# Performance work log

Measured on AMD Instinct MI355X. Metric: run time of the kernel, lower is better.

## Reference

```python
import jax, jax.numpy as jnp
import numpy as np

N = 50000
E = 800000
P = 400000
D_IN = 128
D_HID = 128


def setup_inputs() -> dict:
    key = jax.random.key(0)
    k = jax.random.split(key, 7)
    edge_index = jax.random.randint(k[0], (2, E), 0, N, dtype=jnp.int32)
    edge_pairs = jax.random.randint(k[1], (2, P), 0, N, dtype=jnp.int32)
    emb = jax.random.normal(k[2], (N, D_IN), dtype=jnp.float32)
    W1 = jax.random.normal(k[3], (D_IN, D_HID), dtype=jnp.float32) * (1.0 / np.sqrt(D_IN))
    b1 = jnp.zeros((D_HID,), dtype=jnp.float32)
    W2 = jax.random.normal(k[4], (D_HID, D_HID), dtype=jnp.float32) * (1.0 / np.sqrt(D_HID))
    b2 = jnp.zeros((D_HID,), dtype=jnp.float32)
    return {"edge_index": edge_index, "edge_pairs": edge_pairs, "emb": emb,
            "W1": W1, "b1": b1, "W2": W2, "b2": b2}


def gcn_conv(x, W, b, src, dst):
    """PyG GCNConv: add self-loops, symmetric deg^-1/2 normalization,
    linear transform, scatter-add aggregation into destination nodes."""
    n = x.shape[0]
    loop = jnp.arange(n, dtype=src.dtype)
    s = jnp.concatenate([src, loop])  # [E+N]
    d = jnp.concatenate([dst, loop])
    deg = jax.ops.segment_sum(jnp.ones_like(d, dtype=x.dtype), d, num_segments=n)
    dinv = jnp.where(deg > 0, jax.lax.rsqrt(jnp.maximum(deg, 1e-12)), 0.0)
    norm = dinv[s] * dinv[d]  # [E+N]
    h = x @ W  # [N, out]
    msg = h[s] * norm[:, None]  # gather + scale
    out = jax.ops.segment_sum(msg, d, num_segments=n)  # scatter-add
    return out + b


def reference(edge_index, edge_pairs, emb, W1, b1, W2, b2):
    src, dst = edge_index[0], edge_index[1]
    # encode (eval mode: dropout is identity)
    z = jax.nn.relu(gcn_conv(emb, W1, b1, src, dst))
    z = gcn_conv(z, W2, b2, src, dst)
    # decode: dot product per candidate pair
    return jnp.sum(z[edge_pairs[0]] * z[edge_pairs[1]], axis=1)  # [P]
```

## Files before the change

kernel.cpp:

```cpp
#include <hip/hip_runtime.h>


typedef __attribute__((ext_vector_type(8))) short short8;
typedef __attribute__((ext_vector_type(4))) float floatx4;

#define STAGE_G 128

__device__ __forceinline__ unsigned short f2bf(float f) {
    union { float f; unsigned int u; } v; v.f = f;
    unsigned int u = v.u;
    u += 0x7fffu + ((u >> 16) & 1u);
    return (unsigned short)(u >> 16);
}

__device__ __forceinline__ unsigned int pack2(float a, float b) {
    return (unsigned int)f2bf(a) | ((unsigned int)f2bf(b) << 16);
}

__device__ __forceinline__ float4 cvt4(unsigned int lo, unsigned int hi) {
    float4 f;
    f.x = __uint_as_float(lo << 16);
    f.y = __uint_as_float(lo & 0xffff0000u);
    f.z = __uint_as_float(hi << 16);
    f.w = __uint_as_float(hi & 0xffff0000u);
    return f;
}


__global__ __launch_bounds__(256) void block_hist_kernel(const int* __restrict__ dst,
                                                         int* __restrict__ bhist,
                                                         int E, int NB) {
    __shared__ int bh[1024];
    int t = threadIdx.x, g = blockIdx.x;
    for (int b = t; b < NB; b += 256) bh[b] = 0;
    __syncthreads();
    int chunk = (E + gridDim.x - 1) / gridDim.x;
    int lo = g * chunk, hi = min(lo + chunk, E);
    for (int i = lo + t; i < hi; i += 256) atomicAdd(&bh[dst[i] >> 6], 1);
    __syncthreads();
    for (int b = t; b < NB; b += 256) bhist[g * NB + b] = bh[b];
}

__global__ __launch_bounds__(128) void s1_scan_blocks(int* __restrict__ bhist,
                                                      int* __restrict__ T, int NB) {
    __shared__ int s[2][128];
    int b = blockIdx.x, t = threadIdx.x;
    int v = bhist[t * NB + b];
    int cur = 0;
    s[0][t] = v;
    __syncthreads();
#pragma unroll
    for (int off = 1; off < 128; off <<= 1) {
        int nxt = cur ^ 1;
        int val = s[cur][t];
        if (t >= off) val += s[cur][t - off];
        s[nxt][t] = val;
        __syncthreads();
        cur = nxt;
    }
    int inc = s[cur][t];
    bhist[t * NB + b] = inc - v;
    if (t == 127) T[b] = inc;
}

__global__ __launch_bounds__(256) void stage_kernel(const int* __restrict__ src,
                                                    const int* __restrict__ dst,
                                                    const int* __restrict__ bhist,
                                                    const int* __restrict__ T,
                                                    int* __restrict__ bucket_base,
                                                    unsigned int* __restrict__ stage,
                                                    int E, int NB) {
    __shared__ int lcur[1024];
    __shared__ int sb[2][256];
    int t = threadIdx.x, g = blockIdx.x;

    int b0 = t * 4;
    int v[4];
    int s = 0;
#pragma unroll
    for (int i = 0; i < 4; ++i) {
        int b = b0 + i;
        v[i] = (b < NB) ? T[b] : 0;
        s += v[i];
    }
    int cur = 0;
    sb[0][t] = s;
    __syncthreads();
#pragma unroll
    for (int off = 1; off < 256; off <<= 1) {
        int val = sb[cur][t];
        if (t >= off) val += sb[cur][t - off];
        sb[cur ^ 1][t] = val;
        __syncthreads();
        cur ^= 1;
    }
    int run = sb[cur][t] - s;
#pragma unroll
    for (int i = 0; i < 4; ++i) {
        int b = b0 + i;
        if (b < NB) {
            lcur[b] = run + bhist[(size_t)g * NB + b];
            if (g == 0) bucket_base[b] = run;
        }
        run += v[i];
    }
    if (g == 0 && t == 255) bucket_base[NB] = run;
    __syncthreads();

    int chunk = (E + gridDim.x - 1) / gridDim.x;
    int lo = g * chunk, hi = min(lo + chunk, E);
    for (int i = lo + t; i < hi; i += 256) {
        int d = dst[i];
        int pos = atomicAdd(&lcur[d >> 6], 1);
        stage[pos] = ((unsigned int)src[i] << 6) | (unsigned int)(d & 63);
    }
}

__global__ __launch_bounds__(256) void scatter_gemm_kernel(const unsigned int* __restrict__ stage,
                                                           const int* __restrict__ bucket_base,
                                                           int* __restrict__ row_ptr,
                                                           float* __restrict__ dinv,
                                                           int* __restrict__ srcs_sorted,
                                                           const float* __restrict__ Xv,
                                                           const float* __restrict__ W,
                                                           uint2* __restrict__ H, int N) {
    __shared__ __align__(16) char smem[50176];
    __shared__ int cnt[64];
    __shared__ int lcur[64];
    __shared__ float sdinv[64];
    short* WB = (short*)smem;
    short* XL = (short*)(smem + 32768);
    float* Cst = (float*)smem;

    const int tid = threadIdx.x;
    const int blk = blockIdx.x;

    {
        int t = tid;
        int lo = blk << 6;
        int base = bucket_base[blk], basen = bucket_base[blk + 1];
        if (t < 64) cnt[t] = 0;
        __syncthreads();
        for (int i = base + t; i < basen; i += 256) atomicAdd(&cnt[stage[i] & 63u], 1);
        __syncthreads();
        if (t < 64) {
            int v = cnt[t];
            int inc = v;
#pragma unroll
            for (int off = 1; off < 64; off <<= 1) {
                int x = __shfl_up(inc, off, 64);
                if (t >= off) inc += x;
            }
            int exc = inc - v;
            int node = lo + t;
            float di = rsqrtf((float)(v + 1));
            if (node < N) {
                row_ptr[node] = base + exc;
                dinv[node] = di;
                if (node == N - 1) row_ptr[N] = base + exc + v;
                sdinv[t] = di;
            } else {
                sdinv[t] = 0.f;
            }
            lcur[t] = base + exc;
        }
        __syncthreads();
        for (int i = base + t; i < basen; i += 256) {
            unsigned int rec = stage[i];
            int pos = atomicAdd(&lcur[rec & 63u], 1);
            srcs_sorted[pos] = (int)(rec >> 6);
        }
    }
    __syncthreads();

    {
        const float4* W4 = (const float4*)W;
#pragma unroll
        for (int i = 0; i < 16; ++i) {
            int f = tid + i * 256;
            int k = f >> 5;
            int c4 = f & 31;
            float4 wv = W4[f];
            int kt = k >> 5, q = (k >> 3) & 3, j = k & 7;
            float e[4] = {wv.x, wv.y, wv.z, wv.w};
#pragma unroll
            for (int m = 0; m < 4; ++m) {
                int c = c4 * 4 + m;
                int nt = c >> 4;
                int ln = q * 16 + (c & 15);
                WB[((nt * 4 + kt) * 64 + ln) * 8 + j] = (short)f2bf(e[m]);
            }
        }
    }
    {
#pragma unroll
        for (int i = 0; i < 8; ++i) {
            int f = tid + i * 256;
            int row = f >> 5;
            int c4 = f & 31;
            int gr = min(blk * 64 + row, N - 1);
            float4 xv = ((const float4*)Xv)[(size_t)gr * 32 + c4];
            uint2 u;
            u.x = pack2(xv.x, xv.y);
            u.y = pack2(xv.z, xv.w);
            *(uint2*)&XL[row * 136 + c4 * 4] = u;
        }
    }
    __syncthreads();

    const int w = tid >> 6;
    const int lane = tid & 63;
    const int arow = w * 16 + (lane & 15);
    const int koff = (lane >> 4) * 8;
    short8 a[4];
#pragma unroll
    for (int kt = 0; kt < 4; ++kt)
        a[kt] = *(const short8*)&XL[arow * 136 + kt * 32 + koff];

    floatx4 acc[8];
#pragma unroll
    for (int nt = 0; nt < 8; ++nt) acc[nt] = (floatx4){0.f, 0.f, 0.f, 0.f};

#pragma unroll
    for (int kt = 0; kt < 4; ++kt) {
#pragma unroll
        for (int nt = 0; nt < 8; ++nt) {
            short8 b = *(const short8*)&WB[((nt * 4 + kt) * 64 + lane) * 8];
            acc[nt] = __builtin_amdgcn_mfma_f32_16x16x32_bf16(a[kt], b, acc[nt], 0, 0, 0);
        }
    }
    __syncthreads();

    {
        int q = lane >> 4, cn = lane & 15;
#pragma unroll
        for (int nt = 0; nt < 8; ++nt)
#pragma unroll
            for (int r = 0; r < 4; ++r)
                Cst[(w * 16 + q * 4 + r) * 132 + nt * 16 + cn] = acc[nt][r];
    }
    __syncthreads();
    {
#pragma unroll
        for (int i = 0; i < 8; ++i) {
            int f = tid + i * 256;
            int row = f >> 5;
            int c4 = f & 31;
            int gr = blk * 64 + row;
            if (gr < N) {
                float4 v = *(float4*)&Cst[row * 132 + c4 * 4];
                float di = sdinv[row];
                uint2 o;
                o.x = pack2(v.x * di, v.y * di);
                o.y = pack2(v.z * di, v.w * di);
                H[(size_t)gr * 32 + c4] = o;
            }
        }
    }
}

__global__ __launch_bounds__(256) void gemm_mfma_kernel(const unsigned short* __restrict__ Xv,
                                                        const float* __restrict__ W,
                                                        const float* __restrict__ dinv,
                                                        uint2* __restrict__ H, int N) {
    __shared__ __align__(16) char smem[50176];
    short* WB = (short*)smem;
    short* XL = (short*)(smem + 32768);
    float* Cst = (float*)smem;

    const int tid = threadIdx.x;
    const int w = tid >> 6;
    const int lane = tid & 63;
    const int blk = blockIdx.x;

    {
        const float4* W4 = (const float4*)W;
#pragma unroll
        for (int i = 0; i < 16; ++i) {
            int f = tid + i * 256;
            int k = f >> 5;
            int c4 = f & 31;
            float4 wv = W4[f];
            int kt = k >> 5, q = (k >> 3) & 3, j = k & 7;
            float e[4] = {wv.x, wv.y, wv.z, wv.w};
#pragma unroll
            for (int m = 0; m < 4; ++m) {
                int c = c4 * 4 + m;
                int nt = c >> 4;
                int ln = q * 16 + (c & 15);
                WB[((nt * 4 + kt) * 64 + ln) * 8 + j] = (short)f2bf(e[m]);
            }
        }
    }
    {
#pragma unroll
        for (int i = 0; i < 8; ++i) {
            int f = tid + i * 256;
            int row = f >> 5;
            int c4 = f & 31;
            int gr = min(blk * 64 + row, N - 1);
            uint2 u = ((const uint2*)Xv)[(size_t)gr * 32 + c4];
            *(uint2*)&XL[row * 136 + c4 * 4] = u;
        }
    }
    __syncthreads();

    const int arow = w * 16 + (lane & 15);
    const int koff = (lane >> 4) * 8;
    short8 a[4];
#pragma unroll
    for (int kt = 0; kt < 4; ++kt)
        a[kt] = *(const short8*)&XL[arow * 136 + kt * 32 + koff];

    floatx4 acc[8];
#pragma unroll
    for (int nt = 0; nt < 8; ++nt) acc[nt] = (floatx4){0.f, 0.f, 0.f, 0.f};

#pragma unroll
    for (int kt = 0; kt < 4; ++kt) {
#pragma unroll
        for (int nt = 0; nt < 8; ++nt) {
            short8 b = *(const short8*)&WB[((nt * 4 + kt) * 64 + lane) * 8];
            acc[nt] = __builtin_amdgcn_mfma_f32_16x16x32_bf16(a[kt], b, acc[nt], 0, 0, 0);
        }
    }
    __syncthreads();

    {
        int q = lane >> 4, cn = lane & 15;
#pragma unroll
        for (int nt = 0; nt < 8; ++nt)
#pragma unroll
            for (int r = 0; r < 4; ++r)
                Cst[(w * 16 + q * 4 + r) * 132 + nt * 16 + cn] = acc[nt][r];
    }
    __syncthreads();
    {
#pragma unroll
        for (int i = 0; i < 8; ++i) {
            int f = tid + i * 256;
            int row = f >> 5;
            int c4 = f & 31;
            int gr = blk * 64 + row;
            if (gr < N) {
                float4 v = *(float4*)&Cst[row * 132 + c4 * 4];
                float di = dinv[gr];
                uint2 o;
                o.x = pack2(v.x * di, v.y * di);
                o.y = pack2(v.z * di, v.w * di);
                H[(size_t)gr * 32 + c4] = o;
            }
        }
    }
}

__global__ __launch_bounds__(256) void agg_kernel(const unsigned short* __restrict__ Hp,
                                                  const int* __restrict__ row_ptr,
                                                  const int* __restrict__ srcs,
                                                  const float* __restrict__ dinv,
                                                  const float* __restrict__ bias,
                                                  unsigned short* __restrict__ Z,
                                                  int N, int do_relu) {
    int gw = (int)((blockIdx.x * blockDim.x + threadIdx.x) >> 6);
    int lane = threadIdx.x & 63;
    int q = lane >> 4;
    int hl = lane & 15;
    int n = gw * 4 + q;
    if (n >= N) return;

    const uint4* H4 = (const uint4*)Hp;
    uint4 us = H4[(size_t)n * 16 + hl];
    float4 a0 = cvt4(us.x, us.y);
    float4 a1 = cvt4(us.z, us.w);
    float4 b0 = make_float4(0.f, 0.f, 0.f, 0.f);
    float4 b1 = make_float4(0.f, 0.f, 0.f, 0.f);

    int j = row_ptr[n], end = row_ptr[n + 1];
    for (; j + 7 < end; j += 8) {
        uint4 u0 = H4[(size_t)srcs[j + 0] * 16 + hl];
        uint4 u1 = H4[(size_t)srcs[j + 1] * 16 + hl];
        uint4 u2 = H4[(size_t)srcs[j + 2] * 16 + hl];
        uint4 u3 = H4[(size_t)srcs[j + 3] * 16 + hl];
        uint4 u4 = H4[(size_t)srcs[j + 4] * 16 + hl];
        uint4 u5 = H4[(size_t)srcs[j + 5] * 16 + hl];
        uint4 u6 = H4[(size_t)srcs[j + 6] * 16 + hl];
        uint4 u7 = H4[(size_t)srcs[j + 7] * 16 + hl];
        float4 t;
        t = cvt4(u0.x, u0.y); a0.x += t.x; a0.y += t.y; a0.z += t.z; a0.w += t.w;
        t = cvt4(u0.z, u0.w); a1.x += t.x; a1.y += t.y; a1.z += t.z; a1.w += t.w;
        t = cvt4(u1.x, u1.y); b0.x += t.x; b0.y += t.y; b0.z += t.z; b0.w += t.w;
        t = cvt4(u1.z, u1.w); b1.x += t.x; b1.y += t.y; b1.z += t.z; b1.w += t.w;
        t = cvt4(u2.x, u2.y); a0.x += t.x; a0.y += t.y; a0.z += t.z; a0.w += t.w;
        t = cvt4(u2.z, u2.w); a1.x += t.x; a1.y += t.y; a1.z += t.z; a1.w += t.w;
        t = cvt4(u3.x, u3.y); b0.x += t.x; b0.y += t.y; b0.z += t.z; b0.w += t.w;
        t = cvt4(u3.z, u3.w); b1.x += t.x; b1.y += t.y; b1.z += t.z; b1.w += t.w;
        t = cvt4(u4.x, u4.y); a0.x += t.x; a0.y += t.y; a0.z += t.z; a0.w += t.w;
        t = cvt4(u4.z, u4.w); a1.x += t.x; a1.y += t.y; a1.z += t.z; a1.w += t.w;
        t = cvt4(u5.x, u5.y); b0.x += t.x; b0.y += t.y; b0.z += t.z; b0.w += t.w;
        t = cvt4(u5.z, u5.w); b1.x += t.x; b1.y += t.y; b1.z += t.z; b1.w += t.w;
        t = cvt4(u6.x, u6.y); a0.x += t.x; a0.y += t.y; a0.z += t.z; a0.w += t.w;
        t = cvt4(u6.z, u6.w); a1.x += t.x; a1.y += t.y; a1.z += t.z; a1.w += t.w;
        t = cvt4(u7.x, u7.y); b0.x += t.x; b0.y += t.y; b0.z += t.z; b0.w += t.w;
        t = cvt4(u7.z, u7.w); b1.x += t.x; b1.y += t.y; b1.z += t.z; b1.w += t.w;
    }
    for (; j + 3 < end; j += 4) {
        uint4 u0 = H4[(size_t)srcs[j + 0] * 16 + hl];
        uint4 u1 = H4[(size_t)srcs[j + 1] * 16 + hl];
        uint4 u2 = H4[(size_t)srcs[j + 2] * 16 + hl];
        uint4 u3 = H4[(size_t)srcs[j + 3] * 16 + hl];
        float4 t;
        t = cvt4(u0.x, u0.y); a0.x += t.x; a0.y += t.y; a0.z += t.z; a0.w += t.w;
        t = cvt4(u0.z, u0.w); a1.x += t.x; a1.y += t.y; a1.z += t.z; a1.w += t.w;
        t = cvt4(u1.x, u1.y); b0.x += t.x; b0.y += t.y; b0.z += t.z; b0.w += t.w;
        t = cvt4(u1.z, u1.w); b1.x += t.x; b1.y += t.y; b1.z += t.z; b1.w += t.w;
        t = cvt4(u2.x, u2.y); a0.x += t.x; a0.y += t.y; a0.z += t.z; a0.w += t.w;
        t = cvt4(u2.z, u2.w); a1.x += t.x; a1.y += t.y; a1.z += t.z; a1.w += t.w;
        t = cvt4(u3.x, u3.y); b0.x += t.x; b0.y += t.y; b0.z += t.z; b0.w += t.w;
        t = cvt4(u3.z, u3.w); b1.x += t.x; b1.y += t.y; b1.z += t.z; b1.w += t.w;
    }
    for (; j < end; ++j) {
        uint4 u = H4[(size_t)srcs[j] * 16 + hl];
        float4 t;
        t = cvt4(u.x, u.y); a0.x += t.x; a0.y += t.y; a0.z += t.z; a0.w += t.w;
        t = cvt4(u.z, u.w); a1.x += t.x; a1.y += t.y; a1.z += t.z; a1.w += t.w;
    }
    a0.x += b0.x; a0.y += b0.y; a0.z += b0.z; a0.w += b0.w;
    a1.x += b1.x; a1.y += b1.y; a1.z += b1.z; a1.w += b1.w;

    float di = dinv[n];
    float4 bv0 = ((const float4*)bias)[2 * hl];
    float4 bv1 = ((const float4*)bias)[2 * hl + 1];
    float o0 = di * a0.x + bv0.x, o1 = di * a0.y + bv0.y;
    float o2 = di * a0.z + bv0.z, o3 = di * a0.w + bv0.w;
    float o4 = di * a1.x + bv1.x, o5 = di * a1.y + bv1.y;
    float o6 = di * a1.z + bv1.z, o7 = di * a1.w + bv1.w;
    if (do_relu) {
        o0 = fmaxf(o0, 0.f); o1 = fmaxf(o1, 0.f); o2 = fmaxf(o2, 0.f); o3 = fmaxf(o3, 0.f);
        o4 = fmaxf(o4, 0.f); o5 = fmaxf(o5, 0.f); o6 = fmaxf(o6, 0.f); o7 = fmaxf(o7, 0.f);
    }
    uint4 o;
    o.x = pack2(o0, o1);
    o.y = pack2(o2, o3);
    o.z = pack2(o4, o5);
    o.w = pack2(o6, o7);
    ((uint4*)Z)[(size_t)n * 16 + hl] = o;
}

__global__ __launch_bounds__(256) void decode_kernel(const unsigned short* __restrict__ Z,
                                                     const int* __restrict__ pa,
                                                     const int* __restrict__ pb,
                                                     float* __restrict__ out, int P) {
    int wv = (int)((blockIdx.x * blockDim.x + threadIdx.x) >> 6);
    int lane = threadIdx.x & 63;
    int q = lane >> 4;
    int hl = lane & 15;
    int p0 = wv * 8 + q * 2;
    if (p0 >= P) return;
    const uint4* Z4 = (const uint4*)Z;

    bool two = (p0 + 1 < P);
    int A0 = pa[p0], B0 = pb[p0];
    int A1 = two ? pa[p0 + 1] : A0;
    int B1 = two ? pb[p0 + 1] : B0;
    uint4 ua0 = Z4[(size_t)A0 * 16 + hl];
    uint4 ub0 = Z4[(size_t)B0 * 16 + hl];
    uint4 ua1 = Z4[(size_t)A1 * 16 + hl];
    uint4 ub1 = Z4[(size_t)B1 * 16 + hl];

    float4 xa, xb, ya, yb;
    xa = cvt4(ua0.x, ua0.y); xb = cvt4(ub0.x, ub0.y);
    ya = cvt4(ua0.z, ua0.w); yb = cvt4(ub0.z, ub0.w);
    float v0 = xa.x * xb.x + xa.y * xb.y + xa.z * xb.z + xa.w * xb.w
             + ya.x * yb.x + ya.y * yb.y + ya.z * yb.z + ya.w * yb.w;
    xa = cvt4(ua1.x, ua1.y); xb = cvt4(ub1.x, ub1.y);
    ya = cvt4(ua1.z, ua1.w); yb = cvt4(ub1.z, ub1.w);
    float v1 = xa.x * xb.x + xa.y * xb.y + xa.z * xb.z + xa.w * xb.w
             + ya.x * yb.x + ya.y * yb.y + ya.z * yb.z + ya.w * yb.w;
#pragma unroll
    for (int off = 8; off > 0; off >>= 1) {
        v0 += __shfl_down(v0, off, 16);
        v1 += __shfl_down(v1, off, 16);
    }
    if (hl == 0) {
        out[p0] = v0;
        if (two) out[p0 + 1] = v1;
    }
}

extern "C" void kernel_launch(void* const* d_in, const int* in_sizes, int n_in,
                              void* d_out, int out_size, void* d_ws, size_t ws_size,
                              hipStream_t stream) {
    const int*   edge_index = (const int*)d_in[0];
    const int*   edge_pairs = (const int*)d_in[1];
    const float* emb        = (const float*)d_in[2];
    const float* W1         = (const float*)d_in[3];
    const float* b1         = (const float*)d_in[4];
    const float* W2         = (const float*)d_in[5];
    const float* b2         = (const float*)d_in[6];
    float* out = (float*)d_out;

    int E = in_sizes[0] / 2;
    int P = in_sizes[1] / 2;
    int N = in_sizes[2] / 128;
    int NB = (N + 63) / 64;

    const int* src = edge_index;
    const int* dst = edge_index + E;
    const int* pa  = edge_pairs;
    const int* pb  = edge_pairs + P;

    char* ws = (char*)d_ws;
    size_t off = 0;
    auto alloc = [&](size_t bytes) -> void* {
        void* p = ws + off;
        off = (off + bytes + 255) & ~(size_t)255;
        return p;
    };
    unsigned short* bufA = (unsigned short*)alloc((size_t)N * 128 * 2);
    unsigned short* bufB = (unsigned short*)alloc((size_t)N * 128 * 2);
    int*   srcs_sorted  = (int*)alloc((size_t)E * sizeof(int));
    unsigned int* stage = (unsigned int*)alloc((size_t)E * sizeof(unsigned int));
    int*   row_ptr      = (int*)alloc((size_t)(N + 1) * sizeof(int));
    float* dinv         = (float*)alloc((size_t)N * sizeof(float));
    int*   bhist        = (int*)alloc((size_t)STAGE_G * NB * sizeof(int));
    int*   T            = (int*)alloc((size_t)NB * sizeof(int));
    int*   bucket_base  = (int*)alloc((size_t)(NB + 1) * sizeof(int));

    block_hist_kernel<<<STAGE_G, 256, 0, stream>>>(dst, bhist, E, NB);
    s1_scan_blocks<<<NB, 128, 0, stream>>>(bhist, T, NB);
    stage_kernel<<<STAGE_G, 256, 0, stream>>>(src, dst, bhist, T, bucket_base, stage, E, NB);

    scatter_gemm_kernel<<<NB, 256, 0, stream>>>(stage, bucket_base, row_ptr, dinv,
                                                srcs_sorted, emb, W1, (uint2*)bufA, N);

    agg_kernel<<<(N + 15) / 16, 256, 0, stream>>>(bufA, row_ptr, srcs_sorted, dinv, b1,
                                                  bufB, N, 1);

    gemm_mfma_kernel<<<NB, 256, 0, stream>>>(bufB, W2, dinv, (uint2*)bufA, N);

    agg_kernel<<<(N + 15) / 16, 256, 0, stream>>>(bufA, row_ptr, srcs_sorted, dinv, b2,
                                                  bufB, N, 0);

    decode_kernel<<<(P + 31) / 32, 256, 0, stream>>>(bufB, pa, pb, out, P);
}
```

Measured before the change: 244.8 us.

## Split aggregation and decode into four column-slice passes for cache locality

The aggregation and decode kernels now process the 128-wide bf16 feature rows in four passes of 32 columns each, with four threads per node or pair instead of sixteen. Each pass touches only a quarter of the feature table, so the gathered working set (about 3.2 MB per pass) is more likely to stay resident in L2/MALL during random neighbour gathers. The cost is four times as many launches, repeated reads of row_ptr, srcs and pair indices, and only 64-byte gathers per node per pass. Decode now accumulates into the output across passes with read-modify-write.

```diff
diff --git a/kernel.cpp b/kernel.cpp
--- a/kernel.cpp
+++ b/kernel.cpp
@@ -354,22 +354,20 @@
     }
 }
 
-__global__ __launch_bounds__(256) void agg_kernel(const unsigned short* __restrict__ Hp,
-                                                  const int* __restrict__ row_ptr,
-                                                  const int* __restrict__ srcs,
-                                                  const float* __restrict__ dinv,
-                                                  const float* __restrict__ bias,
-                                                  unsigned short* __restrict__ Z,
-                                                  int N, int do_relu) {
-    int gw = (int)((blockIdx.x * blockDim.x + threadIdx.x) >> 6);
-    int lane = threadIdx.x & 63;
-    int q = lane >> 4;
-    int hl = lane & 15;
-    int n = gw * 4 + q;
+__global__ __launch_bounds__(256) void agg_pass_kernel(const unsigned short* __restrict__ Hp,
+                                                       const int* __restrict__ row_ptr,
+                                                       const int* __restrict__ srcs,
+                                                       const float* __restrict__ dinv,
+                                                       const float* __restrict__ bias,
+                                                       unsigned short* __restrict__ Z,
+                                                       int N, int do_relu, int pass) {
+    int n = (int)((blockIdx.x * blockDim.x + threadIdx.x) >> 2);
+    int sl = threadIdx.x & 3;
     if (n >= N) return;
-
     const uint4* H4 = (const uint4*)Hp;
-    uint4 us = H4[(size_t)n * 16 + hl];
+    const int co = pass * 4 + sl;
+
+    uint4 us = H4[(size_t)n * 16 + co];
     float4 a0 = cvt4(us.x, us.y);
     float4 a1 = cvt4(us.z, us.w);
     float4 b0 = make_float4(0.f, 0.f, 0.f, 0.f);
@@ -377,14 +375,14 @@
 
     int j = row_ptr[n], end = row_ptr[n + 1];
     for (; j + 7 < end; j += 8) {
-        uint4 u0 = H4[(size_t)srcs[j + 0] * 16 + hl];
-        uint4 u1 = H4[(size_t)srcs[j + 1] * 16 + hl];
-        uint4 u2 = H4[(size_t)srcs[j + 2] * 16 + hl];
-        uint4 u3 = H4[(size_t)srcs[j + 3] * 16 + hl];
-        uint4 u4 = H4[(size_t)srcs[j + 4] * 16 + hl];
-        uint4 u5 = H4[(size_t)srcs[j + 5] * 16 + hl];
-        uint4 u6 = H4[(size_t)srcs[j + 6] * 16 + hl];
-        uint4 u7 = H4[(size_t)srcs[j + 7] * 16 + hl];
+        uint4 u0 = H4[(size_t)srcs[j + 0] * 16 + co];
+        uint4 u1 = H4[(size_t)srcs[j + 1] * 16 + co];
+        uint4 u2 = H4[(size_t)srcs[j + 2] * 16 + co];
+        uint4 u3 = H4[(size_t)srcs[j + 3] * 16 + co];
+        uint4 u4 = H4[(size_t)srcs[j + 4] * 16 + co];
+        uint4 u5 = H4[(size_t)srcs[j + 5] * 16 + co];
+        uint4 u6 = H4[(size_t)srcs[j + 6] * 16 + co];
+        uint4 u7 = H4[(size_t)srcs[j + 7] * 16 + co];
         float4 t;
         t = cvt4(u0.x, u0.y); a0.x += t.x; a0.y += t.y; a0.z += t.z; a0.w += t.w;
         t = cvt4(u0.z, u0.w); a1.x += t.x; a1.y += t.y; a1.z += t.z; a1.w += t.w;
@@ -404,10 +402,10 @@
         t = cvt4(u7.z, u7.w); b1.x += t.x; b1.y += t.y; b1.z += t.z; b1.w += t.w;
     }
     for (; j + 3 < end; j += 4) {
-        uint4 u0 = H4[(size_t)srcs[j + 0] * 16 + hl];
-        uint4 u1 = H4[(size_t)srcs[j + 1] * 16 + hl];
-        uint4 u2 = H4[(size_t)srcs[j + 2] * 16 + hl];
-        uint4 u3 = H4[(size_t)srcs[j + 3] * 16 + hl];
+        uint4 u0 = H4[(size_t)srcs[j + 0] * 16 + co];
+        uint4 u1 = H4[(size_t)srcs[j + 1] * 16 + co];
+        uint4 u2 = H4[(size_t)srcs[j + 2] * 16 + co];
+        uint4 u3 = H4[(size_t)srcs[j + 3] * 16 + co];
         float4 t;
         t = cvt4(u0.x, u0.y); a0.x += t.x; a0.y += t.y; a0.z += t.z; a0.w += t.w;
         t = cvt4(u0.z, u0.w); a1.x += t.x; a1.y += t.y; a1.z += t.z; a1.w += t.w;
@@ -419,7 +417,7 @@
         t = cvt4(u3.z, u3.w); b1.x += t.x; b1.y += t.y; b1.z += t.z; b1.w += t.w;
     }
     for (; j < end; ++j) {
-        uint4 u = H4[(size_t)srcs[j] * 16 + hl];
+        uint4 u = H4[(size_t)srcs[j] * 16 + co];
         float4 t;
         t = cvt4(u.x, u.y); a0.x += t.x; a0.y += t.y; a0.z += t.z; a0.w += t.w;
         t = cvt4(u.z, u.w); a1.x += t.x; a1.y += t.y; a1.z += t.z; a1.w += t.w;
@@ -428,8 +426,8 @@
     a1.x += b1.x; a1.y += b1.y; a1.z += b1.z; a1.w += b1.w;
 
     float di = dinv[n];
-    float4 bv0 = ((const float4*)bias)[2 * hl];
-    float4 bv1 = ((const float4*)bias)[2 * hl + 1];
+    float4 bv0 = ((const float4*)bias)[2 * co];
+    float4 bv1 = ((const float4*)bias)[2 * co + 1];
     float o0 = di * a0.x + bv0.x, o1 = di * a0.y + bv0.y;
     float o2 = di * a0.z + bv0.z, o3 = di * a0.w + bv0.w;
     float o4 = di * a1.x + bv1.x, o5 = di * a1.y + bv1.y;
@@ -443,47 +441,33 @@
     o.y = pack2(o2, o3);
     o.z = pack2(o4, o5);
     o.w = pack2(o6, o7);
-    ((uint4*)Z)[(size_t)n * 16 + hl] = o;
-}
-
-__global__ __launch_bounds__(256) void decode_kernel(const unsigned short* __restrict__ Z,
-                                                     const int* __restrict__ pa,
-                                                     const int* __restrict__ pb,
-                                                     float* __restrict__ out, int P) {
-    int wv = (int)((blockIdx.x * blockDim.x + threadIdx.x) >> 6);
-    int lane = threadIdx.x & 63;
-    int q = lane >> 4;
-    int hl = lane & 15;
-    int p0 = wv * 8 + q * 2;
-    if (p0 >= P) return;
-    const uint4* Z4 = (const uint4*)Z;
-
-    bool two = (p0 + 1 < P);
-    int A0 = pa[p0], B0 = pb[p0];
-    int A1 = two ? pa[p0 + 1] : A0;
-    int B1 = two ? pb[p0 + 1] : B0;
-    uint4 ua0 = Z4[(size_t)A0 * 16 + hl];
-    uint4 ub0 = Z4[(size_t)B0 * 16 + hl];
-    uint4 ua1 = Z4[(size_t)A1 * 16 + hl];
-    uint4 ub1 = Z4[(size_t)B1 * 16 + hl];
-
-    float4 xa, xb, ya, yb;
-    xa = cvt4(ua0.x, ua0.y); xb = cvt4(ub0.x, ub0.y);
-    ya = cvt4(ua0.z, ua0.w); yb = cvt4(ub0.z, ub0.w);
-    float v0 = xa.x * xb.x + xa.y * xb.y + xa.z * xb.z + xa.w * xb.w
-             + ya.x * yb.x + ya.y * yb.y + ya.z * yb.z + ya.w * yb.w;
-    xa = cvt4(ua1.x, ua1.y); xb = cvt4(ub1.x, ub1.y);
-    ya = cvt4(ua1.z, ua1.w); yb = cvt4(ub1.z, ub1.w);
-    float v1 = xa.x * xb.x + xa.y * xb.y + xa.z * xb.z + xa.w * xb.w
-             + ya.x * yb.x + ya.y * yb.y + ya.z * yb.z + ya.w * yb.w;
-#pragma unroll
-    for (int off = 8; off > 0; off >>= 1) {
-        v0 += __shfl_down(v0, off, 16);
-        v1 += __shfl_down(v1, off, 16);
-    }
-    if (hl == 0) {
-        out[p0] = v0;
-        if (two) out[p0 + 1] = v1;
+    ((uint4*)Z)[(size_t)n * 16 + co] = o;
+}
+
+__global__ __launch_bounds__(256) void decode_pass_kernel(const unsigned short* __restrict__ Zp,
+                                                          const int* __restrict__ pa,
+                                                          const int* __restrict__ pb,
+                                                          float* __restrict__ out,
+                                                          int P, int pass) {
+    int pr = (int)((blockIdx.x * blockDim.x + threadIdx.x) >> 2);
+    int sl = threadIdx.x & 3;
+    if (pr >= P) return;
+    const uint4* Z4 = (const uint4*)Zp;
+    const int co = pass * 4 + sl;
+
+    int A = pa[pr], B = pb[pr];
+    uint4 ua = Z4[(size_t)A * 16 + co];
+    uint4 ub = Z4[(size_t)B * 16 + co];
+
+    float4 xa = cvt4(ua.x, ua.y), ya = cvt4(ua.z, ua.w);
+    float4 xb = cvt4(ub.x, ub.y), yb = cvt4(ub.z, ub.w);
+    float v = xa.x * xb.x + xa.y * xb.y + xa.z * xb.z + xa.w * xb.w
+            + ya.x * yb.x + ya.y * yb.y + ya.z * yb.z + ya.w * yb.w;
+    v += __shfl_xor(v, 1, 4);
+    v += __shfl_xor(v, 2, 4);
+    if (sl == 0) {
+        if (pass == 0) out[pr] = v;
+        else out[pr] += v;
     }
 }
 
@@ -533,13 +517,19 @@
     scatter_gemm_kernel<<<NB, 256, 0, stream>>>(stage, bucket_base, row_ptr, dinv,
                                                 srcs_sorted, emb, W1, (uint2*)bufA, N);
 
-    agg_kernel<<<(N + 15) / 16, 256, 0, stream>>>(bufA, row_ptr, srcs_sorted, dinv, b1,
-                                                  bufB, N, 1);
+    int aggB = (N + 63) / 64;
+    int decB = (P + 63) / 64;
+
+    for (int p = 0; p < 4; ++p)
+        agg_pass_kernel<<<aggB, 256, 0, stream>>>(bufA, row_ptr, srcs_sorted, dinv, b1,
+                                                  bufB, N, 1, p);
 
     gemm_mfma_kernel<<<NB, 256, 0, stream>>>(bufB, W2, dinv, (uint2*)bufA, N);
 
-    agg_kernel<<<(N + 15) / 16, 256, 0, stream>>>(bufA, row_ptr, srcs_sorted, dinv, b2,
-                                                  bufB, N, 0);
-
-    decode_kernel<<<(P + 31) / 32, 256, 0, stream>>>(bufB, pa, pb, out, P);
-}
+    for (int p = 0; p < 4; ++p)
+        agg_pass_kernel<<<aggB, 256, 0, stream>>>(bufA, row_ptr, srcs_sorted, dinv, b2,
+                                                  bufB, N, 0, p);
+
+    for (int p = 0; p < 4; ++p)
+        decode_pass_kernel<<<decB, 256, 0, stream>>>(bufB, pa, pb, out, P, p);
+}
```

Result: slower. 312.4 us (+27.6%).

## Bucket decode pairs by source node and precompute bf16 weight layouts once

Applied to the files above, without the earlier changes.

The decode step now bucket-sorts candidate pairs by their first endpoint, reusing the histogram/scan/stage pipeline already used for edges. Each decode block loads its 64-row tile of Z into shared memory once and reads the A-side rows from LDS, so only the B-side rows are gathered from global memory. Separately, W1 and W2 are converted to the MFMA-friendly bf16 layout once in the histogram kernel and simply copied by each GEMM block, instead of every block repeating the conversion. This adds extra histogram, scan and stage work over the P pairs plus scattered output writes, in exchange for fewer random Z gathers.

```diff
diff --git a/kernel.cpp b/kernel.cpp
--- a/kernel.cpp
+++ b/kernel.cpp
@@ -28,84 +28,180 @@
 
 
 __global__ __launch_bounds__(256) void block_hist_kernel(const int* __restrict__ dst,
+                                                         const int* __restrict__ pa,
                                                          int* __restrict__ bhist,
-                                                         int E, int NB) {
+                                                         int* __restrict__ phist,
+                                                         const float* __restrict__ W1,
+                                                         const float* __restrict__ W2,
+                                                         short* __restrict__ wb1,
+                                                         short* __restrict__ wb2,
+                                                         int E, int P, int NB) {
     __shared__ int bh[1024];
+    __shared__ int bh2[1024];
     int t = threadIdx.x, g = blockIdx.x;
-    for (int b = t; b < NB; b += 256) bh[b] = 0;
+
+    if (g < 32) {
+        const float4* W4 = (const float4*)((g < 16) ? W1 : W2);
+        short* wb = (g < 16) ? wb1 : wb2;
+        int f = ((g & 15) * 256) + t;
+        int k = f >> 5;
+        int c4 = f & 31;
+        float4 wv = W4[f];
+        int kt = k >> 5, q = (k >> 3) & 3, j = k & 7;
+        float e[4] = {wv.x, wv.y, wv.z, wv.w};
+#pragma unroll
+        for (int m = 0; m < 4; ++m) {
+            int c = c4 * 4 + m;
+            int nt = c >> 4;
+            int ln = q * 16 + (c & 15);
+            wb[((nt * 4 + kt) * 64 + ln) * 8 + j] = (short)f2bf(e[m]);
+        }
+    }
+
+    for (int b = t; b < NB; b += 256) { bh[b] = 0; bh2[b] = 0; }
     __syncthreads();
     int chunk = (E + gridDim.x - 1) / gridDim.x;
     int lo = g * chunk, hi = min(lo + chunk, E);
     for (int i = lo + t; i < hi; i += 256) atomicAdd(&bh[dst[i] >> 6], 1);
-    __syncthreads();
-    for (int b = t; b < NB; b += 256) bhist[g * NB + b] = bh[b];
+    int chunkP = (P + gridDim.x - 1) / gridDim.x;
+    int loP = g * chunkP, hiP = min(loP + chunkP, P);
+    for (int i = loP + t; i < hiP; i += 256) atomicAdd(&bh2[pa[i] >> 6], 1);
+    __syncthreads();
+    for (int b = t; b < NB; b += 256) {
+        bhist[g * NB + b] = bh[b];
+        phist[g * NB + b] = bh2[b];
+    }
 }
 
 __global__ __launch_bounds__(128) void s1_scan_blocks(int* __restrict__ bhist,
-                                                      int* __restrict__ T, int NB) {
+                                                      int* __restrict__ phist,
+                                                      int* __restrict__ T,
+                                                      int* __restrict__ T2, int NB) {
     __shared__ int s[2][128];
     int b = blockIdx.x, t = threadIdx.x;
-    int v = bhist[t * NB + b];
-    int cur = 0;
-    s[0][t] = v;
-    __syncthreads();
-#pragma unroll
-    for (int off = 1; off < 128; off <<= 1) {
-        int nxt = cur ^ 1;
-        int val = s[cur][t];
-        if (t >= off) val += s[cur][t - off];
-        s[nxt][t] = val;
-        __syncthreads();
-        cur = nxt;
-    }
-    int inc = s[cur][t];
-    bhist[t * NB + b] = inc - v;
-    if (t == 127) T[b] = inc;
+    {
+        int v = bhist[t * NB + b];
+        int cur = 0;
+        s[0][t] = v;
+        __syncthreads();
+#pragma unroll
+        for (int off = 1; off < 128; off <<= 1) {
+            int nxt = cur ^ 1;
+            int val = s[cur][t];
+            if (t >= off) val += s[cur][t - off];
+            s[nxt][t] = val;
+            __syncthreads();
+            cur = nxt;
+        }
+        int inc = s[cur][t];
+        bhist[t * NB + b] = inc - v;
+        if (t == 127) T[b] = inc;
+        __syncthreads();
+    }
+    {
+        int v = phist[t * NB + b];
+        int cur = 0;
+        s[0][t] = v;
+        __syncthreads();
+#pragma unroll
+        for (int off = 1; off < 128; off <<= 1) {
+            int nxt = cur ^ 1;
+            int val = s[cur][t];
+            if (t >= off) val += s[cur][t - off];
+            s[nxt][t] = val;
+            __syncthreads();
+            cur = nxt;
+        }
+        int inc = s[cur][t];
+        phist[t * NB + b] = inc - v;
+        if (t == 127) T2[b] = inc;
+    }
 }
 
 __global__ __launch_bounds__(256) void stage_kernel(const int* __restrict__ src,
                                                     const int* __restrict__ dst,
+                                                    const int* __restrict__ pa,
                                                     const int* __restrict__ bhist,
+                                                    const int* __restrict__ phist,
                                                     const int* __restrict__ T,
+                                                    const int* __restrict__ T2,
                                                     int* __restrict__ bucket_base,
+                                                    int* __restrict__ pair_base,
                                                     unsigned int* __restrict__ stage,
-                                                    int E, int NB) {
+                                                    unsigned int* __restrict__ stageP,
+                                                    int E, int P, int NB) {
     __shared__ int lcur[1024];
+    __shared__ int lcur2[1024];
     __shared__ int sb[2][256];
     int t = threadIdx.x, g = blockIdx.x;
 
     int b0 = t * 4;
-    int v[4];
-    int s = 0;
-#pragma unroll
-    for (int i = 0; i < 4; ++i) {
-        int b = b0 + i;
-        v[i] = (b < NB) ? T[b] : 0;
-        s += v[i];
-    }
-    int cur = 0;
-    sb[0][t] = s;
-    __syncthreads();
-#pragma unroll
-    for (int off = 1; off < 256; off <<= 1) {
-        int val = sb[cur][t];
-        if (t >= off) val += sb[cur][t - off];
-        sb[cur ^ 1][t] = val;
-        __syncthreads();
-        cur ^= 1;
-    }
-    int run = sb[cur][t] - s;
-#pragma unroll
-    for (int i = 0; i < 4; ++i) {
-        int b = b0 + i;
-        if (b < NB) {
-            lcur[b] = run + bhist[(size_t)g * NB + b];
-            if (g == 0) bucket_base[b] = run;
-        }
-        run += v[i];
-    }
-    if (g == 0 && t == 255) bucket_base[NB] = run;
-    __syncthreads();
+    {
+        int v[4];
+        int s = 0;
+#pragma unroll
+        for (int i = 0; i < 4; ++i) {
+            int b = b0 + i;
+            v[i] = (b < NB) ? T[b] : 0;
+            s += v[i];
+        }
+        int cur = 0;
+        sb[0][t] = s;
+        __syncthreads();
+#pragma unroll
+        for (int off = 1; off < 256; off <<= 1) {
+            int val = sb[cur][t];
+            if (t >= off) val += sb[cur][t - off];
+            sb[cur ^ 1][t] = val;
+            __syncthreads();
+            cur ^= 1;
+        }
+        int run = sb[cur][t] - s;
+#pragma unroll
+        for (int i = 0; i < 4; ++i) {
+            int b = b0 + i;
+            if (b < NB) {
+                lcur[b] = run + bhist[(size_t)g * NB + b];
+                if (g == 0) bucket_base[b] = run;
+            }
+            run += v[i];
+        }
+        if (g == 0 && t == 255) bucket_base[NB] = run;
+        __syncthreads();
+    }
+    {
+        int v[4];
+        int s = 0;
+#pragma unroll
+        for (int i = 0; i < 4; ++i) {
+            int b = b0 + i;
+            v[i] = (b < NB) ? T2[b] : 0;
+            s += v[i];
+        }
+        int cur = 0;
+        sb[0][t] = s;
+        __syncthreads();
+#pragma unroll
+        for (int off = 1; off < 256; off <<= 1) {
+            int val = sb[cur][t];
+            if (t >= off) val += sb[cur][t - off];
+            sb[cur ^ 1][t] = val;
+            __syncthreads();
+            cur ^= 1;
+        }
+        int run = sb[cur][t] - s;
+#pragma unroll
+        for (int i = 0; i < 4; ++i) {
+            int b = b0 + i;
+            if (b < NB) {
+                lcur2[b] = run + phist[(size_t)g * NB + b];
+                if (g == 0) pair_base[b] = run;
+            }
+            run += v[i];
+        }
+        if (g == 0 && t == 255) pair_base[NB] = run;
+        __syncthreads();
+    }
 
     int chunk = (E + gridDim.x - 1) / gridDim.x;
     int lo = g * chunk, hi = min(lo + chunk, E);
@@ -114,6 +210,13 @@
         int pos = atomicAdd(&lcur[d >> 6], 1);
         stage[pos] = ((unsigned int)src[i] << 6) | (unsigned int)(d & 63);
     }
+    int chunkP = (P + gridDim.x - 1) / gridDim.x;
+    int loP = g * chunkP, hiP = min(loP + chunkP, P);
+    for (int i = loP + t; i < hiP; i += 256) {
+        int A = pa[i];
+        int pos = atomicAdd(&lcur2[A >> 6], 1);
+        stageP[pos] = ((unsigned int)i << 6) | (unsigned int)(A & 63);
+    }
 }
 
 __global__ __launch_bounds__(256) void scatter_gemm_kernel(const unsigned int* __restrict__ stage,
@@ -122,7 +225,7 @@
                                                            float* __restrict__ dinv,
                                                            int* __restrict__ srcs_sorted,
                                                            const float* __restrict__ Xv,
-                                                           const float* __restrict__ W,
+                                                           const short* __restrict__ wbpre,
                                                            uint2* __restrict__ H, int N) {
     __shared__ __align__(16) char smem[50176];
     __shared__ int cnt[64];
@@ -174,22 +277,12 @@
     __syncthreads();
 
     {
-        const float4* W4 = (const float4*)W;
-#pragma unroll
-        for (int i = 0; i < 16; ++i) {
-            int f = tid + i * 256;
-            int k = f >> 5;
-            int c4 = f & 31;
-            float4 wv = W4[f];
-            int kt = k >> 5, q = (k >> 3) & 3, j = k & 7;
-            float e[4] = {wv.x, wv.y, wv.z, wv.w};
-#pragma unroll
-            for (int m = 0; m < 4; ++m) {
-                int c = c4 * 4 + m;
-                int nt = c >> 4;
-                int ln = q * 16 + (c & 15);
-                WB[((nt * 4 + kt) * 64 + ln) * 8 + j] = (short)f2bf(e[m]);
-            }
+        const uint4* Wp = (const uint4*)wbpre;
+        uint4* WB4 = (uint4*)WB;
+#pragma unroll
+        for (int i = 0; i < 8; ++i) {
+            int idx = tid + i * 256;
+            WB4[idx] = Wp[idx];
         }
     }
     {
@@ -260,7 +353,7 @@
 }
 
 __global__ __launch_bounds__(256) void gemm_mfma_kernel(const unsigned short* __restrict__ Xv,
-                                                        const float* __restrict__ W,
+                                                        const short* __restrict__ wbpre,
                                                         const float* __restrict__ dinv,
                                                         uint2* __restrict__ H, int N) {
     __shared__ __align__(16) char smem[50176];
@@ -274,22 +367,12 @@
     const int blk = blockIdx.x;
 
     {
-        const float4* W4 = (const float4*)W;
-#pragma unroll
-        for (int i = 0; i < 16; ++i) {
-            int f = tid + i * 256;
-            int k = f >> 5;
-            int c4 = f & 31;
-            float4 wv = W4[f];
-            int kt = k >> 5, q = (k >> 3) & 3, j = k & 7;
-            float e[4] = {wv.x, wv.y, wv.z, wv.w};
-#pragma unroll
-            for (int m = 0; m < 4; ++m) {
-                int c = c4 * 4 + m;
-                int nt = c >> 4;
-                int ln = q * 16 + (c & 15);
-                WB[((nt * 4 + kt) * 64 + ln) * 8 + j] = (short)f2bf(e[m]);
-            }
+        const uint4* Wp = (const uint4*)wbpre;
+        uint4* WB4 = (uint4*)WB;
+#pragma unroll
+        for (int i = 0; i < 8; ++i) {
+            int idx = tid + i * 256;
+            WB4[idx] = Wp[idx];
         }
     }
     {
@@ -446,44 +529,80 @@
     ((uint4*)Z)[(size_t)n * 16 + hl] = o;
 }
 
-__global__ __launch_bounds__(256) void decode_kernel(const unsigned short* __restrict__ Z,
-                                                     const int* __restrict__ pa,
-                                                     const int* __restrict__ pb,
-                                                     float* __restrict__ out, int P) {
-    int wv = (int)((blockIdx.x * blockDim.x + threadIdx.x) >> 6);
-    int lane = threadIdx.x & 63;
-    int q = lane >> 4;
-    int hl = lane & 15;
-    int p0 = wv * 8 + q * 2;
-    if (p0 >= P) return;
-    const uint4* Z4 = (const uint4*)Z;
-
-    bool two = (p0 + 1 < P);
-    int A0 = pa[p0], B0 = pb[p0];
-    int A1 = two ? pa[p0 + 1] : A0;
-    int B1 = two ? pb[p0 + 1] : B0;
-    uint4 ua0 = Z4[(size_t)A0 * 16 + hl];
-    uint4 ub0 = Z4[(size_t)B0 * 16 + hl];
-    uint4 ua1 = Z4[(size_t)A1 * 16 + hl];
-    uint4 ub1 = Z4[(size_t)B1 * 16 + hl];
-
-    float4 xa, xb, ya, yb;
-    xa = cvt4(ua0.x, ua0.y); xb = cvt4(ub0.x, ub0.y);
-    ya = cvt4(ua0.z, ua0.w); yb = cvt4(ub0.z, ub0.w);
-    float v0 = xa.x * xb.x + xa.y * xb.y + xa.z * xb.z + xa.w * xb.w
-             + ya.x * yb.x + ya.y * yb.y + ya.z * yb.z + ya.w * yb.w;
-    xa = cvt4(ua1.x, ua1.y); xb = cvt4(ub1.x, ub1.y);
-    ya = cvt4(ua1.z, ua1.w); yb = cvt4(ub1.z, ub1.w);
-    float v1 = xa.x * xb.x + xa.y * xb.y + xa.z * xb.z + xa.w * xb.w
-             + ya.x * yb.x + ya.y * yb.y + ya.z * yb.z + ya.w * yb.w;
-#pragma unroll
-    for (int off = 8; off > 0; off >>= 1) {
-        v0 += __shfl_down(v0, off, 16);
-        v1 += __shfl_down(v1, off, 16);
-    }
-    if (hl == 0) {
-        out[p0] = v0;
-        if (two) out[p0 + 1] = v1;
+__global__ __launch_bounds__(256) void decode_bucket_kernel(const unsigned short* __restrict__ Zp,
+                                                            const unsigned int* __restrict__ stageP,
+                                                            const int* __restrict__ pair_base,
+                                                            const int* __restrict__ pb,
+                                                            float* __restrict__ out,
+                                                            int N) {
+    __shared__ __align__(16) short AL[64 * 136];
+    const int tid = threadIdx.x;
+    const int blk = blockIdx.x >> 1;
+    const int half = blockIdx.x & 1;
+    const uint4* Z4 = (const uint4*)Zp;
+
+#pragma unroll
+    for (int i = 0; i < 4; ++i) {
+        int idx = tid + i * 256;
+        int row = idx >> 4, hl = idx & 15;
+        int gr = min(blk * 64 + row, N - 1);
+        *(uint4*)&AL[row * 136 + hl * 8] = Z4[(size_t)gr * 16 + hl];
+    }
+    __syncthreads();
+
+    int base = pair_base[blk], basen = pair_base[blk + 1];
+    int gp = half * 16 + (tid >> 4);
+    int hl = tid & 15;
+
+    for (int k = base + gp; k < basen; k += 128) {
+        int i1 = k + 32, i2 = k + 64, i3 = k + 96;
+        bool h1 = i1 < basen, h2 = i2 < basen, h3 = i3 < basen;
+        unsigned r0 = stageP[k];
+        unsigned r1 = h1 ? stageP[i1] : r0;
+        unsigned r2 = h2 ? stageP[i2] : r0;
+        unsigned r3 = h3 ? stageP[i3] : r0;
+        int p0 = (int)(r0 >> 6), p1 = (int)(r1 >> 6);
+        int p2 = (int)(r2 >> 6), p3 = (int)(r3 >> 6);
+        int B0 = pb[p0], B1 = pb[p1], B2 = pb[p2], B3 = pb[p3];
+        uint4 ub0 = Z4[(size_t)B0 * 16 + hl];
+        uint4 ub1 = Z4[(size_t)B1 * 16 + hl];
+        uint4 ub2 = Z4[(size_t)B2 * 16 + hl];
+        uint4 ub3 = Z4[(size_t)B3 * 16 + hl];
+        uint4 ua0 = *(const uint4*)&AL[(int)(r0 & 63u) * 136 + hl * 8];
+        uint4 ua1 = *(const uint4*)&AL[(int)(r1 & 63u) * 136 + hl * 8];
+        uint4 ua2 = *(const uint4*)&AL[(int)(r2 & 63u) * 136 + hl * 8];
+        uint4 ua3 = *(const uint4*)&AL[(int)(r3 & 63u) * 136 + hl * 8];
+
+        float4 xa, xb, ya, yb;
+        xa = cvt4(ua0.x, ua0.y); xb = cvt4(ub0.x, ub0.y);
+        ya = cvt4(ua0.z, ua0.w); yb = cvt4(ub0.z, ub0.w);
+        float v0 = xa.x * xb.x + xa.y * xb.y + xa.z * xb.z + xa.w * xb.w
+                 + ya.x * yb.x + ya.y * yb.y + ya.z * yb.z + ya.w * yb.w;
+        xa = cvt4(ua1.x, ua1.y); xb = cvt4(ub1.x, ub1.y);
+        ya = cvt4(ua1.z, ua1.w); yb = cvt4(ub1.z, ub1.w);
+        float v1 = xa.x * xb.x + xa.y * xb.y + xa.z * xb.z + xa.w * xb.w
+                 + ya.x * yb.x + ya.y * yb.y + ya.z * yb.z + ya.w * yb.w;
+        xa = cvt4(ua2.x, ua2.y); xb = cvt4(ub2.x, ub2.y);
+        ya = cvt4(ua2.z, ua2.w); yb = cvt4(ub2.z, ub2.w);
+        float v2 = xa.x * xb.x + xa.y * xb.y + xa.z * xb.z + xa.w * xb.w
+                 + ya.x * yb.x + ya.y * yb.y + ya.z * yb.z + ya.w * yb.w;
+        xa = cvt4(ua3.x, ua3.y); xb = cvt4(ub3.x, ub3.y);
+        ya = cvt4(ua3.z, ua3.w); yb = cvt4(ub3.z, ub3.w);
+        float v3 = xa.x * xb.x + xa.y * xb.y + xa.z * xb.z + xa.w * xb.w
+                 + ya.x * yb.x + ya.y * yb.y + ya.z * yb.z + ya.w * yb.w;
+#pragma unroll
+        for (int off = 8; off > 0; off >>= 1) {
+            v0 += __shfl_down(v0, off, 16);
+            v1 += __shfl_down(v1, off, 16);
+            v2 += __shfl_down(v2, off, 16);
+            v3 += __shfl_down(v3, off, 16);
+        }
+        if (hl == 0) {
+            out[p0] = v0;
+            if (h1) out[p1] = v1;
+            if (h2) out[p2] = v2;
+            if (h3) out[p3] = v3;
+        }
     }
 }
 
@@ -525,21 +644,30 @@
     int*   bhist        = (int*)alloc((size_t)STAGE_G * NB * sizeof(int));
     int*   T            = (int*)alloc((size_t)NB * sizeof(int));
     int*   bucket_base  = (int*)alloc((size_t)(NB + 1) * sizeof(int));
-
-    block_hist_kernel<<<STAGE_G, 256, 0, stream>>>(dst, bhist, E, NB);
-    s1_scan_blocks<<<NB, 128, 0, stream>>>(bhist, T, NB);
-    stage_kernel<<<STAGE_G, 256, 0, stream>>>(src, dst, bhist, T, bucket_base, stage, E, NB);
+    int*   phist        = (int*)alloc((size_t)STAGE_G * NB * sizeof(int));
+    int*   T2           = (int*)alloc((size_t)NB * sizeof(int));
+    int*   pair_base    = (int*)alloc((size_t)(NB + 1) * sizeof(int));
+    unsigned int* stageP = (unsigned int*)alloc((size_t)P * sizeof(unsigned int));
+    short* wb1          = (short*)alloc((size_t)16384 * sizeof(short));
+    short* wb2          = (short*)alloc((size_t)16384 * sizeof(short));
+
+    block_hist_kernel<<<STAGE_G, 256, 0, stream>>>(dst, pa, bhist, phist, W1, W2,
+                                                   wb1, wb2, E, P, NB);
+    s1_scan_blocks<<<NB, 128, 0, stream>>>(bhist, phist, T, T2, NB);
+    stage_kernel<<<STAGE_G, 256, 0, stream>>>(src, dst, pa, bhist, phist, T, T2,
+                                              bucket_base, pair_base, stage, stageP,
+                                              E, P, NB);
 
     scatter_gemm_kernel<<<NB, 256, 0, stream>>>(stage, bucket_base, row_ptr, dinv,
-                                                srcs_sorted, emb, W1, (uint2*)bufA, N);
+                                                srcs_sorted, emb, wb1, (uint2*)bufA, N);
 
     agg_kernel<<<(N + 15) / 16, 256, 0, stream>>>(bufA, row_ptr, srcs_sorted, dinv, b1,
                                                   bufB, N, 1);
 
-    gemm_mfma_kernel<<<NB, 256, 0, stream>>>(bufB, W2, dinv, (uint2*)bufA, N);
+    gemm_mfma_kernel<<<NB, 256, 0, stream>>>(bufB, wb2, dinv, (uint2*)bufA, N);
 
     agg_kernel<<<(N + 15) / 16, 256, 0, stream>>>(bufA, row_ptr, srcs_sorted, dinv, b2,
                                                   bufB, N, 0);
 
-    decode_kernel<<<(P + 31) / 32, 256, 0, stream>>>(bufB, pa, pb, out, P);
-}
+    decode_bucket_kernel<<<NB * 2, 256, 0, stream>>>(bufB, stageP, pair_base, pb, out, N);
+}
```

Measured after the change: 254.2 us. 3.8% more time.
